# Optimization experiments

Measured on AMD Instinct MI355X. Metric: run time of the kernel, lower is better.

Reference implementation:

```python
import jax, jax.numpy as jnp
from jax import lax
import numpy as np

MAX_D = 4  # max_displacement


def conv3x3(x, w, b):
    # x: [B,Cin,H,W], w: [Cout,Cin,3,3], SAME padding (pad=1)
    y = lax.conv_general_dilated(
        x, w, window_strides=(1, 1), padding='SAME',
        dimension_numbers=('NCHW', 'OIHW', 'NCHW'))
    return y + b[None, :, None, None]


def compute_cost_volume(f1, f2, d):
    # roll+mask in the torch code == shift with zero padding:
    # cv[idx,h,w] = mean_c f1[c,h,w] * f2[c,h-i,w-j] (zero outside bounds)
    B, C, H, W = f1.shape
    pad = jnp.pad(f2, ((0, 0), (0, 0), (d, d), (d, d)))
    slices = []
    for i in range(-d, d + 1):
        for j in range(-d, d + 1):
            shifted = lax.dynamic_slice(pad, (0, 0, d - i, d - j), (B, C, H, W))
            slices.append((f1 * shifted).sum(axis=1) / C)  # [B,H,W]
    return jnp.stack(slices, axis=1)  # [B,81,H,W]


def setup_inputs() -> dict:
    key = jax.random.key(0)
    ks = jax.random.split(key, 10)
    B, C, H, W = 16, 64, 128, 128
    cv_ch = (2 * MAX_D + 1) ** 2  # 81
    def w_init(k, shape):
        fan_in = shape[1] * shape[2] * shape[3]
        return jax.random.normal(k, shape, dtype=jnp.float32) * np.float32(np.sqrt(2.0 / fan_in))
    return {
        'f1': jax.random.normal(ks[0], (B, C, H, W), dtype=jnp.float32),
        'f2_warped': jax.random.normal(ks[1], (B, C, H, W), dtype=jnp.float32),
        'w1': w_init(ks[2], (128, C + cv_ch, 3, 3)),
        'b1': jnp.zeros((128,), dtype=jnp.float32),
        'w2': w_init(ks[3], (64, 128, 3, 3)),
        'b2': jnp.zeros((64,), dtype=jnp.float32),
        'w3': w_init(ks[4], (32, 64, 3, 3)),
        'b3': jnp.zeros((32,), dtype=jnp.float32),
        'w4': w_init(ks[5], (2, 32, 3, 3)),
        'b4': jnp.zeros((2,), dtype=jnp.float32),
    }


def reference(f1, f2_warped, w1, b1, w2, b2, w3, b3, w4, b4):
    cv = compute_cost_volume(f1, f2_warped, MAX_D)       # [B,81,H,W]
    x = jnp.concatenate([f1, cv], axis=1)                # [B,145,H,W]
    x = jax.nn.relu(conv3x3(x, w1, b1))
    x = jax.nn.relu(conv3x3(x, w2, b2))
    x = jax.nn.relu(conv3x3(x, w3, b3))
    flow = conv3x3(x, w4, b4)                            # [B,2,H,W]
    return flow
```

## Files before the change

### kernel.cpp

```cpp
#include <hip/hip_runtime.h>


typedef __bf16 bf16x8 __attribute__((ext_vector_type(8)));
typedef float f32x4 __attribute__((ext_vector_type(4)));

__device__ __forceinline__ unsigned short f2bf_bits(float f) {
  unsigned int u = __float_as_uint(f);
  unsigned int r = (u + 0x7FFFu + ((u >> 16) & 1u)) >> 16;
  return (unsigned short)r;
}

__device__ __forceinline__ void glds16(const ushort* gp, ushort* lp) {
  __builtin_amdgcn_global_load_lds((const __attribute__((address_space(1))) void*)gp,
                                   (__attribute__((address_space(3))) void*)lp, 16, 0, 0);
}

__global__ void prep_w_kernel(const float* __restrict__ w, uint4* __restrict__ wp,
                              int CIN, int COUT, int CHUNKS, int NFRAG) {
  int idx = blockIdx.x * 256 + threadIdx.x;
  int total = CHUNKS * 9 * NFRAG * 64;
  if (idx >= total) return;
  int lane = idx & 63;
  int fi = idx >> 6;
  int nf = fi % NFRAG;
  int t = fi / NFRAG;
  int rs = t % 9;
  int c = t / 9;
  int co = nf * 16 + (lane & 15);
  int cib = c * 32 + (lane >> 4) * 8;
  union { uint4 q; ushort s[8]; } pk;
#pragma unroll
  for (int e = 0; e < 8; ++e) {
    int ci = cib + e;
    float v = (ci < CIN && co < COUT) ? w[(co * CIN + ci) * 9 + rs] : 0.f;
    pk.s[e] = f2bf_bits(v);
  }
  wp[idx] = pk.q;
}

__global__ __launch_bounds__(256) void pack_f1_kernel(const float* __restrict__ f1,
                                                      ushort* __restrict__ xf1) {
  __shared__ float tile[64][132];
  const int bid = blockIdx.x;
  const int h = bid & 127, b = bid >> 7;
  const int tid = threadIdx.x;
  for (int e = tid; e < 64 * 128; e += 256) {
    int c = e >> 7, w = e & 127;
    tile[c][w] = f1[((b * 64 + c) * 128 + h) * 128 + w];
  }
  __syncthreads();
  const int px = tid >> 1, cgb = (tid & 1) * 4;
  const long base = ((long)(b * 128 + h) * 128 + px) * 64;
#pragma unroll
  for (int e = 0; e < 4; ++e) {
    int c0 = (cgb + e) * 8;
    union { uint4 q; ushort s[8]; } pk;
#pragma unroll
    for (int k = 0; k < 8; ++k) pk.s[k] = f2bf_bits(tile[c0 + k][px]);
    *reinterpret_cast<uint4*>(&xf1[base + c0]) = pk.q;
  }
}

__global__ __launch_bounds__(256)
void cost_volume_kernel(const float* __restrict__ f1,
                        const float* __restrict__ f2,
                        ushort* __restrict__ xcv) {
  const int bx = blockIdx.x;
  const int idx = bx >> 3;
  const int b = 2 * (bx & 7) + (idx >> 6);
  const int h0 = (idx & 63) * 2;
  const int tid = threadIdx.x;
  const int q = tid & 31;
  const int rho = (tid >> 5) & 1;
  const int g = tid >> 6;

  __shared__ float arena[6464];

  float accF[2][9][4];
  float accP[3][4];
#pragma unroll
  for (int s = 0; s < 2; ++s)
#pragma unroll
    for (int jj = 0; jj < 9; ++jj)
#pragma unroll
      for (int e = 0; e < 4; ++e) accF[s][jj][e] = 0.f;
#pragma unroll
  for (int t = 0; t < 3; ++t)
#pragma unroll
    for (int e = 0; e < 4; ++e) accP[t][e] = 0.f;

  float st[13];

  auto stage = [&](int c) {
    const int cc = c * 2;
#pragma unroll
    for (int i = 0; i < 13; ++i) {
      int e = tid + i * 256;
      float v = 0.f;
      if (e < 2720) {
        int ci = e / 1360;
        int rem = e - ci * 1360;
        int a = rem / 136;
        int k = rem - a * 136;
        int gh = h0 - 4 + a, gw = k - 4;
        if ((unsigned)gh < 128u && (unsigned)gw < 128u)
          v = f2[((b * 64 + cc + ci) * 128 + gh) * 128 + gw];
      } else if (e < 3232) {
        int e2 = e - 2720;
        int ci = e2 >> 8, rr = (e2 >> 7) & 1, ww = e2 & 127;
        v = f1[((b * 64 + cc + ci) * 128 + h0 + rr) * 128 + ww];
      }
      st[i] = v;
    }
  };
  auto commit = [&](int bi) {
    float* bufp = arena + bi * 3232;
#pragma unroll
    for (int i = 0; i < 13; ++i) {
      int e = tid + i * 256;
      if (e < 3232) bufp[e] = st[i];
    }
  };

  stage(0);
  commit(0);

  for (int c = 0; c < 32; ++c) {
    __syncthreads();
    if (c < 31) stage(c + 1);
    const float* bufc = arena + (c & 1) * 3232;
#pragma unroll
    for (int ci = 0; ci < 2; ++ci) {
      const float* bp = bufc + ci * 1360;
      float4 f1q = *reinterpret_cast<const float4*>(bufc + 2720 + ci * 256 + rho * 128 + 4 * q);
      const float* f1e = &f1q.x;
#pragma unroll
      for (int s = 0; s < 2; ++s) {
        int a = rho + 8 - (2 * g + s);
        const float* rp = bp + a * 136 + 4 * q;
        float4 A = *reinterpret_cast<const float4*>(rp);
        float4 Bv = *reinterpret_cast<const float4*>(rp + 4);
        float4 Cv = *reinterpret_cast<const float4*>(rp + 8);
        float ev[12] = {A.x, A.y, A.z, A.w, Bv.x, Bv.y, Bv.z, Bv.w, Cv.x, Cv.y, Cv.z, Cv.w};
#pragma unroll
        for (int jj = 0; jj < 9; ++jj)
#pragma unroll
          for (int e = 0; e < 4; ++e)
            accF[s][jj][e] += f1e[e] * ev[8 - jj + e];
      }
      {
        const float* rp = bp + rho * 136 + 4 * q;
        if (g < 2) {
          float4 A = *reinterpret_cast<const float4*>(rp + 4);
          float4 Bv = *reinterpret_cast<const float4*>(rp + 8);
          float pv[8] = {A.x, A.y, A.z, A.w, Bv.x, Bv.y, Bv.z, Bv.w};
          if (g == 0) {
#pragma unroll
            for (int e = 0; e < 4; ++e) {
              accP[0][e] += f1e[e] * pv[4 + e];
              accP[1][e] += f1e[e] * pv[3 + e];
              accP[2][e] += f1e[e] * pv[2 + e];
            }
          } else {
#pragma unroll
            for (int e = 0; e < 4; ++e) {
              accP[0][e] += f1e[e] * pv[1 + e];
              accP[1][e] += f1e[e] * pv[e];
            }
          }
        } else {
          float4 A = *reinterpret_cast<const float4*>(rp);
          float4 Bv = *reinterpret_cast<const float4*>(rp + 4);
          float pv[8] = {A.x, A.y, A.z, A.w, Bv.x, Bv.y, Bv.z, Bv.w};
          if (g == 2) {
#pragma unroll
            for (int e = 0; e < 4; ++e) {
              accP[0][e] += f1e[e] * pv[3 + e];
              accP[1][e] += f1e[e] * pv[2 + e];
            }
          } else {
#pragma unroll
            for (int e = 0; e < 4; ++e) {
              accP[0][e] += f1e[e] * pv[1 + e];
              accP[1][e] += f1e[e] * pv[e];
            }
          }
        }
      }
    }
    if (c < 31) commit((c + 1) & 1);
  }

  ushort* sO = (ushort*)arena;
  const float inv = 1.0f / 64.0f;
#pragma unroll
  for (int r = 0; r < 2; ++r) {
    __syncthreads();
    if (rho == r) {
#pragma unroll
      for (int s = 0; s < 2; ++s) {
        int ch = (2 * g + s) * 9;
#pragma unroll
        for (int jj = 0; jj < 9; ++jj) {
          uint lo = (uint)f2bf_bits(accF[s][jj][0] * inv) | ((uint)f2bf_bits(accF[s][jj][1] * inv) << 16);
          uint hi = (uint)f2bf_bits(accF[s][jj][2] * inv) | ((uint)f2bf_bits(accF[s][jj][3] * inv) << 16);
          ushort* d = &sO[(ch + jj) * 132 + 4 * q];
          *reinterpret_cast<uint*>(d) = lo;
          *reinterpret_cast<uint*>(d + 2) = hi;
        }
      }
      const int npart = (g == 0) ? 3 : 2;
      const int chbase = 72 + ((g == 0) ? 0 : (g == 1) ? 3 : (g == 2) ? 5 : 7);
#pragma unroll
      for (int t = 0; t < 3; ++t) {
        if (t < npart) {
          uint lo = (uint)f2bf_bits(accP[t][0] * inv) | ((uint)f2bf_bits(accP[t][1] * inv) << 16);
          uint hi = (uint)f2bf_bits(accP[t][2] * inv) | ((uint)f2bf_bits(accP[t][3] * inv) << 16);
          ushort* d = &sO[(chbase + t) * 132 + 4 * q];
          *reinterpret_cast<uint*>(d) = lo;
          *reinterpret_cast<uint*>(d + 2) = hi;
        }
      }
    }
    if (r == 0) {
      for (int e = tid; e < 960; e += 256) {
        int ch = 81 + (e >> 6);
        int pxh = e & 63;
        *reinterpret_cast<uint*>(&sO[ch * 132 + pxh * 2]) = 0u;
      }
    }
    __syncthreads();
    uint4* dst = reinterpret_cast<uint4*>(xcv + ((long)(b * 128 + h0 + r) * 128) * 96);
#pragma unroll
    for (int j = 0; j < 6; ++j) {
      int t8 = 256 * j + tid;
      int px = t8 / 12;
      int ch0 = (t8 - px * 12) * 8;
      union { uint4 qq; ushort ss[8]; } pk;
#pragma unroll
      for (int k = 0; k < 8; ++k) pk.ss[k] = sO[(ch0 + k) * 132 + px];
      dst[t8] = pk.qq;
    }
  }
}

template <int CA, int CB, int COUT, bool RELU, bool PLANAR>
__global__ __launch_bounds__(512, 2)
void conv_mfma_kernel(const ushort* __restrict__ xa, const ushort* __restrict__ xb,
                      const uint4* __restrict__ wp, const float* __restrict__ bias,
                      void* __restrict__ outv) {
  constexpr int CHUNKS = (CA + CB) / 32;
  constexpr int NFRAG = COUT / 16;
  constexpr int NFW = (NFRAG >= 2) ? NFRAG / 2 : 1;
  constexpr int MFW = (NFRAG >= 2) ? 4 : 2;
  constexpr int SXN = 4 * 130 * 32;
  constexpr int WTQ = 9 * NFRAG * 64;
  constexpr int WI = (WTQ + 511) / 512;
  constexpr int SO_STRIDE = COUT + 4;
  constexpr int STAGE_B = PLANAR ? 2048 : 2 * 128 * SO_STRIDE * 2;
  constexpr int SX_B = 2 * SXN * 2;
  constexpr int BASE_B = SX_B + WTQ * 16;
  constexpr int ARENA_B = STAGE_B > BASE_B ? STAGE_B : BASE_B;

  __shared__ __align__(16) char arena[ARENA_B];
  ushort* sXa = (ushort*)arena;
  ushort* sWt = (ushort*)(arena + SX_B);

  const int bx = blockIdx.x;
  const int idx = bx >> 3;
  const int b = 2 * (bx & 7) + (idx >> 6);
  const int h0 = (idx & 63) * 2;
  const int tid = threadIdx.x;
  const int lane = tid & 63;
  const int wid = tid >> 6;
  const int l15 = lane & 15;
  const int lg = lane >> 4;
  const int cg    = (NFRAG >= 2) ? (wid >> 2) : 0;
  const int row   = (NFRAG >= 2) ? ((wid >> 1) & 1) : (wid >> 2);
  const int pbase = (NFRAG >= 2) ? ((wid & 1) * 64) : ((wid & 3) * 32);

  f32x4 acc[MFW][NFW];
#pragma unroll
  for (int mf = 0; mf < MFW; ++mf)
#pragma unroll
    for (int nf = 0; nf < NFW; ++nf) acc[mf][nf] = {0.f, 0.f, 0.f, 0.f};

  if (tid < 64) {
    int bi = tid >> 5, tr = (tid >> 3) & 3, wz = (tid >> 2) & 1, gq = tid & 3;
    int wl = wz ? 129 : 0;
    *reinterpret_cast<uint4*>(&sXa[bi * SXN + ((tr * 130 + wl) * 4 + gq) * 8]) =
        make_uint4(0u, 0u, 0u, 0u);
  }
  if (h0 == 0 || h0 == 126) {
    const int trz = (h0 == 0) ? 0 : 3;
#pragma unroll
    for (int e = 0; e < 2; ++e) {
      int u = tid + e * 512;
      int bi = u >> 9, k = u & 511;
      *reinterpret_cast<uint4*>(&sXa[bi * SXN + ((trz * 130 + 1) * 4 + k) * 8]) =
          make_uint4(0u, 0u, 0u, 0u);
    }
  }

  auto stage = [&](int c, int bi) {
    const int c0 = c * 32;
    const ushort* src;
    int cst, coff;
    if (CB == 0 || c0 < CA) { src = xa; cst = CA; coff = c0; }
    else                    { src = xb; cst = CB; coff = c0 - CA; }
    const int tr = wid >> 1;
    const int gh = h0 - 1 + tr;
    if ((unsigned)gh < 128u) {
      const ushort* rowp = src + ((long)(b * 128 + gh) * 128) * cst + coff;
#pragma unroll
      for (int t = 0; t < 4; ++t) {
        int s = (wid & 1) * 4 + t;
        int u = s * 64 + lane;
        int wl = 1 + (u >> 2);
        int gq = lane & 3;
        int sw = (wl + (wl >> 2)) & 3;
        const ushort* gp = rowp + (long)(wl - 1) * cst + (gq ^ sw) * 8;
        ushort* lp = &sXa[bi * SXN + ((tr * 130 + 1) * 4 + s * 64) * 8];
        glds16(gp, lp);
      }
    }
  };

  auto stage_wt = [&](int c) {
    const ushort* src = (const ushort*)(wp + (size_t)c * WTQ);
#pragma unroll
    for (int i = 0; i < WI; ++i) {
      int e = tid + i * 512;
      if ((WTQ & 511) == 0 || e < WTQ)
        glds16(src + e * 8, sWt + (size_t)(tid & ~63) * 8 + (size_t)(i * 512) * 8);
    }
  };

  stage(0, 0);
  stage_wt(0);
  __syncthreads();

  for (int c = 0; c < CHUNKS; ++c) {
    if (c + 1 < CHUNKS) stage(c + 1, (c + 1) & 1);
    const int bi = c & 1;
#pragma unroll
    for (int rs = 0; rs < 9; ++rs) {
      const int r = rs / 3, s = rs % 3;
      const int tr = row + r;
      bf16x8 afr[MFW];
#pragma unroll
      for (int mf = 0; mf < MFW; ++mf) {
        int wl = pbase + mf * 16 + l15 + s;
        int sw = (wl + (wl >> 2)) & 3;
        afr[mf] = *reinterpret_cast<const bf16x8*>(
            &sXa[bi * SXN + ((tr * 130 + wl) * 4 + (lg ^ sw)) * 8]);
      }
      const ushort* wrow = sWt + (size_t)(rs * NFRAG + cg * NFW) * 64 * 8;
#pragma unroll
      for (int nf = 0; nf < NFW; ++nf) {
        bf16x8 bfr = *reinterpret_cast<const bf16x8*>(wrow + (nf * 64 + lane) * 8);
#pragma unroll
        for (int mf = 0; mf < MFW; ++mf)
          acc[mf][nf] = __builtin_amdgcn_mfma_f32_16x16x32_bf16(afr[mf], bfr, acc[mf][nf], 0, 0, 0);
      }
    }
    __syncthreads();
    if (c + 1 < CHUNKS) stage_wt(c + 1);
    __syncthreads();
  }

  if (!PLANAR) {
    ushort* sO = (ushort*)arena;
#pragma unroll
    for (int nf = 0; nf < NFW; ++nf) {
      float bs = bias[cg * NFW * 16 + nf * 16 + l15];
#pragma unroll
      for (int mf = 0; mf < MFW; ++mf) {
        int px2 = row * 128 + pbase + mf * 16 + lg * 4;
#pragma unroll
        for (int j = 0; j < 4; ++j) {
          float v = acc[mf][nf][j] + bs;
          if (RELU) v = fmaxf(v, 0.f);
          sO[(px2 + j) * SO_STRIDE + cg * NFW * 16 + nf * 16 + l15] = f2bf_bits(v);
        }
      }
    }
    __syncthreads();
    constexpr int QPP = COUT / 8;
    uint4* dst = reinterpret_cast<uint4*>((ushort*)outv + ((long)(b * 128 + h0) * 128) * COUT);
#pragma unroll
    for (int t0 = 0; t0 < 2 * 128 * QPP / 512; ++t0) {
      int t = t0 * 512 + tid;
      int px2 = t / QPP;
      int ch0 = (t & (QPP - 1)) * 8;
      union { uint4 qq; ushort ss[8]; } pk;
#pragma unroll
      for (int k = 0; k < 8; ++k) pk.ss[k] = sO[px2 * SO_STRIDE + ch0 + k];
      dst[t] = pk.qq;
    }
  } else {
    float* sF = (float*)arena;
    if (l15 < 2) {
#pragma unroll
      for (int mf = 0; mf < MFW; ++mf) {
        int pxb = pbase + mf * 16 + lg * 4;
#pragma unroll
        for (int j = 0; j < 4; ++j)
          sF[(l15 * 2 + row) * 128 + pxb + j] = acc[mf][0][j] + bias[l15];
      }
    }
    __syncthreads();
    float* out = (float*)outv;
    if (tid < 128) {
      int ch = tid >> 6, r = (tid >> 5) & 1, qx = tid & 31;
      *reinterpret_cast<float4*>(&out[((long)(b * 2 + ch) * 128 + h0 + r) * 128 + qx * 4]) =
          *reinterpret_cast<float4*>(&sF[(ch * 2 + r) * 128 + qx * 4]);
    }
  }
}

extern "C" void kernel_launch(void* const* d_in, const int* in_sizes, int n_in,
                              void* d_out, int out_size, void* d_ws, size_t ws_size,
                              hipStream_t stream) {
  (void)in_sizes; (void)n_in; (void)out_size; (void)ws_size;
  const float* f1 = (const float*)d_in[0];
  const float* f2 = (const float*)d_in[1];
  const float* w1 = (const float*)d_in[2];
  const float* b1 = (const float*)d_in[3];
  const float* w2 = (const float*)d_in[4];
  const float* b2 = (const float*)d_in[5];
  const float* w3 = (const float*)d_in[6];
  const float* b3 = (const float*)d_in[7];
  const float* w4 = (const float*)d_in[8];
  const float* b4 = (const float*)d_in[9];

  char* ws = (char*)d_ws;
  size_t off = 0;
  ushort* xf1 = (ushort*)(ws + off); off += (size_t)262144 * 64 * 2;
  ushort* xcv = (ushort*)(ws + off); off += (size_t)262144 * 96 * 2;
  ushort* x1  = (ushort*)(ws + off); off += (size_t)262144 * 128 * 2;
  ushort* x2  = (ushort*)(ws + off); off += (size_t)262144 * 64 * 2;
  uint4* wp1 = (uint4*)(ws + off); off += (size_t)5 * 9 * 8 * 64 * 16;
  uint4* wp2 = (uint4*)(ws + off); off += (size_t)4 * 9 * 4 * 64 * 16;
  uint4* wp3 = (uint4*)(ws + off); off += (size_t)2 * 9 * 2 * 64 * 16;
  uint4* wp4 = (uint4*)(ws + off); off += (size_t)1 * 9 * 1 * 64 * 16;
  ushort* x3 = xf1;

  prep_w_kernel<<<90, 256, 0, stream>>>(w1, wp1, 145, 128, 5, 8);
  prep_w_kernel<<<36, 256, 0, stream>>>(w2, wp2, 128, 64, 4, 4);
  prep_w_kernel<<<9, 256, 0, stream>>>(w3, wp3, 64, 32, 2, 2);
  prep_w_kernel<<<3, 256, 0, stream>>>(w4, wp4, 32, 2, 1, 1);

  pack_f1_kernel<<<2048, 256, 0, stream>>>(f1, xf1);
  cost_volume_kernel<<<1024, 256, 0, stream>>>(f1, f2, xcv);

  conv_mfma_kernel<64, 96, 128, true, false><<<1024, 512, 0, stream>>>(xf1, xcv, wp1, b1, x1);
  conv_mfma_kernel<128, 0, 64, true, false><<<1024, 512, 0, stream>>>(x1, x1, wp2, b2, x2);
  conv_mfma_kernel<64, 0, 32, true, false><<<1024, 512, 0, stream>>>(x2, x2, wp3, b3, x3);
  conv_mfma_kernel<32, 0, 16, false, true><<<1024, 512, 0, stream>>>(x3, x3, wp4, b4, d_out);
}
```

Before: 335.4 us.

## Compute cost volume with bf16 MFMA on packed NHWC f1/f2

```diff
diff --git a/kernel.cpp b/kernel.cpp
--- a/kernel.cpp
+++ b/kernel.cpp
@@ -62,185 +62,99 @@
 }
 
 __global__ __launch_bounds__(256)
-void cost_volume_kernel(const float* __restrict__ f1,
-                        const float* __restrict__ f2,
-                        ushort* __restrict__ xcv) {
+void cost_volume_mfma_kernel(const ushort* __restrict__ xf1,
+                             const ushort* __restrict__ xf2,
+                             ushort* __restrict__ xcv) {
   const int bx = blockIdx.x;
   const int idx = bx >> 3;
-  const int b = 2 * (bx & 7) + (idx >> 6);
-  const int h0 = (idx & 63) * 2;
+  const int b = 2 * (bx & 7) + (idx >> 7);
+  const int h = idx & 127;
   const int tid = threadIdx.x;
-  const int q = tid & 31;
-  const int rho = (tid >> 5) & 1;
+  const int lane = tid & 63;
   const int g = tid >> 6;
-
-  __shared__ float arena[6464];
-
-  float accF[2][9][4];
-  float accP[3][4];
-#pragma unroll
-  for (int s = 0; s < 2; ++s)
-#pragma unroll
-    for (int jj = 0; jj < 9; ++jj)
-#pragma unroll
-      for (int e = 0; e < 4; ++e) accF[s][jj][e] = 0.f;
-#pragma unroll
-  for (int t = 0; t < 3; ++t)
-#pragma unroll
-    for (int e = 0; e < 4; ++e) accP[t][e] = 0.f;
-
-  float st[13];
-
-  auto stage = [&](int c) {
-    const int cc = c * 2;
-#pragma unroll
-    for (int i = 0; i < 13; ++i) {
-      int e = tid + i * 256;
-      float v = 0.f;
-      if (e < 2720) {
-        int ci = e / 1360;
-        int rem = e - ci * 1360;
-        int a = rem / 136;
-        int k = rem - a * 136;
-        int gh = h0 - 4 + a, gw = k - 4;
-        if ((unsigned)gh < 128u && (unsigned)gw < 128u)
-          v = f2[((b * 64 + cc + ci) * 128 + gh) * 128 + gw];
-      } else if (e < 3232) {
-        int e2 = e - 2720;
-        int ci = e2 >> 8, rr = (e2 >> 7) & 1, ww = e2 & 127;
-        v = f1[((b * 64 + cc + ci) * 128 + h0 + rr) * 128 + ww];
-      }
-      st[i] = v;
-    }
-  };
-  auto commit = [&](int bi) {
-    float* bufp = arena + bi * 3232;
-#pragma unroll
-    for (int i = 0; i < 13; ++i) {
-      int e = tid + i * 256;
-      if (e < 3232) bufp[e] = st[i];
-    }
-  };
-
-  stage(0);
-  commit(0);
-
-  for (int c = 0; c < 32; ++c) {
-    __syncthreads();
-    if (c < 31) stage(c + 1);
-    const float* bufc = arena + (c & 1) * 3232;
-#pragma unroll
-    for (int ci = 0; ci < 2; ++ci) {
-      const float* bp = bufc + ci * 1360;
-      float4 f1q = *reinterpret_cast<const float4*>(bufc + 2720 + ci * 256 + rho * 128 + 4 * q);
-      const float* f1e = &f1q.x;
-#pragma unroll
-      for (int s = 0; s < 2; ++s) {
-        int a = rho + 8 - (2 * g + s);
-        const float* rp = bp + a * 136 + 4 * q;
-        float4 A = *reinterpret_cast<const float4*>(rp);
-        float4 Bv = *reinterpret_cast<const float4*>(rp + 4);
-        float4 Cv = *reinterpret_cast<const float4*>(rp + 8);
-        float ev[12] = {A.x, A.y, A.z, A.w, Bv.x, Bv.y, Bv.z, Bv.w, Cv.x, Cv.y, Cv.z, Cv.w};
-#pragma unroll
-        for (int jj = 0; jj < 9; ++jj)
-#pragma unroll
-          for (int e = 0; e < 4; ++e)
-            accF[s][jj][e] += f1e[e] * ev[8 - jj + e];
-      }
-      {
-        const float* rp = bp + rho * 136 + 4 * q;
-        if (g < 2) {
-          float4 A = *reinterpret_cast<const float4*>(rp + 4);
-          float4 Bv = *reinterpret_cast<const float4*>(rp + 8);
-          float pv[8] = {A.x, A.y, A.z, A.w, Bv.x, Bv.y, Bv.z, Bv.w};
-          if (g == 0) {
-#pragma unroll
-            for (int e = 0; e < 4; ++e) {
-              accP[0][e] += f1e[e] * pv[4 + e];
-              accP[1][e] += f1e[e] * pv[3 + e];
-              accP[2][e] += f1e[e] * pv[2 + e];
-            }
-          } else {
-#pragma unroll
-            for (int e = 0; e < 4; ++e) {
-              accP[0][e] += f1e[e] * pv[1 + e];
-              accP[1][e] += f1e[e] * pv[e];
-            }
-          }
-        } else {
-          float4 A = *reinterpret_cast<const float4*>(rp);
-          float4 Bv = *reinterpret_cast<const float4*>(rp + 4);
-          float pv[8] = {A.x, A.y, A.z, A.w, Bv.x, Bv.y, Bv.z, Bv.w};
-          if (g == 2) {
-#pragma unroll
-            for (int e = 0; e < 4; ++e) {
-              accP[0][e] += f1e[e] * pv[3 + e];
-              accP[1][e] += f1e[e] * pv[2 + e];
-            }
-          } else {
-#pragma unroll
-            for (int e = 0; e < 4; ++e) {
-              accP[0][e] += f1e[e] * pv[1 + e];
-              accP[1][e] += f1e[e] * pv[e];
-            }
-          }
+  const int l15 = lane & 15;
+  const int lg = lane >> 4;
+
+  __shared__ __align__(16) float sC[4][2][16][33];
+  __shared__ __align__(16) ushort sO[96][132];
+
+  {
+    uint4 z = make_uint4(0u, 0u, 0u, 0u);
+    uint4* p = (uint4*)sO;
+#pragma unroll
+    for (int j = 0; j < 7; ++j) {
+      int e = tid + j * 256;
+      if (e < 1584) p[e] = z;
+    }
+  }
+  __syncthreads();
+
+  const int w0g = g * 32;
+  bf16x8 afr[2][2];
+  {
+    const ushort* f1p = xf1 + ((long)(b * 128 + h) * 128) * 64;
+#pragma unroll
+    for (int wt = 0; wt < 2; ++wt)
+#pragma unroll
+      for (int kc = 0; kc < 2; ++kc) {
+        int pix = w0g + wt * 16 + l15;
+        afr[wt][kc] = *reinterpret_cast<const bf16x8*>(f1p + pix * 64 + kc * 32 + lg * 8);
+      }
+  }
+
+  const float inv = 1.0f / 64.0f;
+  for (int A = 0; A < 9; ++A) {
+    int fr = h - 4 + A;
+    if ((unsigned)fr >= 128u) continue;
+    const ushort* f2p = xf2 + ((long)(b * 128 + fr) * 128) * 64;
+    bf16x8 bfr[3][2];
+#pragma unroll
+    for (int t = 0; t < 3; ++t)
+#pragma unroll
+      for (int kc = 0; kc < 2; ++kc) {
+        int p = w0g - 4 + t * 16 + l15;
+        uint4 v = make_uint4(0u, 0u, 0u, 0u);
+        if ((unsigned)p < 128u)
+          v = *reinterpret_cast<const uint4*>(f2p + (long)p * 64 + kc * 32 + lg * 8);
+        bfr[t][kc] = __builtin_bit_cast(bf16x8, v);
+      }
+#pragma unroll
+    for (int wt = 0; wt < 2; ++wt)
+#pragma unroll
+      for (int nt = 0; nt < 2; ++nt) {
+        f32x4 acc = {0.f, 0.f, 0.f, 0.f};
+        acc = __builtin_amdgcn_mfma_f32_16x16x32_bf16(afr[wt][0], bfr[wt + nt][0], acc, 0, 0, 0);
+        acc = __builtin_amdgcn_mfma_f32_16x16x32_bf16(afr[wt][1], bfr[wt + nt][1], acc, 0, 0, 0);
+#pragma unroll
+        for (int j = 0; j < 4; ++j)
+          sC[g][wt][lg * 4 + j][nt * 16 + l15] = acc[j];
+      }
+    const int chb = (8 - A) * 9;
+#pragma unroll
+    for (int wt = 0; wt < 2; ++wt) {
+      int px = w0g + wt * 16 + l15;
+#pragma unroll
+      for (int u = 0; u < 3; ++u) {
+        if (u < ((lg == 3) ? 3 : 2)) {
+          int tj = lg * 2 + u;
+          float v = sC[g][wt][l15][l15 + 8 - tj];
+          sO[chb + tj][px] = f2bf_bits(v * inv);
         }
       }
     }
-    if (c < 31) commit((c + 1) & 1);
-  }
-
-  ushort* sO = (ushort*)arena;
-  const float inv = 1.0f / 64.0f;
-#pragma unroll
-  for (int r = 0; r < 2; ++r) {
-    __syncthreads();
-    if (rho == r) {
-#pragma unroll
-      for (int s = 0; s < 2; ++s) {
-        int ch = (2 * g + s) * 9;
-#pragma unroll
-        for (int jj = 0; jj < 9; ++jj) {
-          uint lo = (uint)f2bf_bits(accF[s][jj][0] * inv) | ((uint)f2bf_bits(accF[s][jj][1] * inv) << 16);
-          uint hi = (uint)f2bf_bits(accF[s][jj][2] * inv) | ((uint)f2bf_bits(accF[s][jj][3] * inv) << 16);
-          ushort* d = &sO[(ch + jj) * 132 + 4 * q];
-          *reinterpret_cast<uint*>(d) = lo;
-          *reinterpret_cast<uint*>(d + 2) = hi;
-        }
-      }
-      const int npart = (g == 0) ? 3 : 2;
-      const int chbase = 72 + ((g == 0) ? 0 : (g == 1) ? 3 : (g == 2) ? 5 : 7);
-#pragma unroll
-      for (int t = 0; t < 3; ++t) {
-        if (t < npart) {
-          uint lo = (uint)f2bf_bits(accP[t][0] * inv) | ((uint)f2bf_bits(accP[t][1] * inv) << 16);
-          uint hi = (uint)f2bf_bits(accP[t][2] * inv) | ((uint)f2bf_bits(accP[t][3] * inv) << 16);
-          ushort* d = &sO[(chbase + t) * 132 + 4 * q];
-          *reinterpret_cast<uint*>(d) = lo;
-          *reinterpret_cast<uint*>(d + 2) = hi;
-        }
-      }
-    }
-    if (r == 0) {
-      for (int e = tid; e < 960; e += 256) {
-        int ch = 81 + (e >> 6);
-        int pxh = e & 63;
-        *reinterpret_cast<uint*>(&sO[ch * 132 + pxh * 2]) = 0u;
-      }
-    }
-    __syncthreads();
-    uint4* dst = reinterpret_cast<uint4*>(xcv + ((long)(b * 128 + h0 + r) * 128) * 96);
-#pragma unroll
-    for (int j = 0; j < 6; ++j) {
-      int t8 = 256 * j + tid;
-      int px = t8 / 12;
-      int ch0 = (t8 - px * 12) * 8;
-      union { uint4 qq; ushort ss[8]; } pk;
-#pragma unroll
-      for (int k = 0; k < 8; ++k) pk.ss[k] = sO[(ch0 + k) * 132 + px];
-      dst[t8] = pk.qq;
-    }
+  }
+  __syncthreads();
+
+  uint4* dst = reinterpret_cast<uint4*>(xcv + ((long)(b * 128 + h) * 128) * 96);
+#pragma unroll
+  for (int j = 0; j < 6; ++j) {
+    int t8 = j * 256 + tid;
+    int px = t8 / 12;
+    int ch0 = (t8 - px * 12) * 8;
+    union { uint4 qq; ushort ss[8]; } pk;
+#pragma unroll
+    for (int k = 0; k < 8; ++k) pk.ss[k] = sO[ch0 + k][px];
+    dst[t8] = pk.qq;
   }
 }
 
@@ -444,7 +358,8 @@
   uint4* wp2 = (uint4*)(ws + off); off += (size_t)4 * 9 * 4 * 64 * 16;
   uint4* wp3 = (uint4*)(ws + off); off += (size_t)2 * 9 * 2 * 64 * 16;
   uint4* wp4 = (uint4*)(ws + off); off += (size_t)1 * 9 * 1 * 64 * 16;
-  ushort* x3 = xf1;
+  ushort* x3  = xf1;
+  ushort* xf2 = x1;
 
   prep_w_kernel<<<90, 256, 0, stream>>>(w1, wp1, 145, 128, 5, 8);
   prep_w_kernel<<<36, 256, 0, stream>>>(w2, wp2, 128, 64, 4, 4);
@@ -452,7 +367,8 @@
   prep_w_kernel<<<3, 256, 0, stream>>>(w4, wp4, 32, 2, 1, 1);
 
   pack_f1_kernel<<<2048, 256, 0, stream>>>(f1, xf1);
-  cost_volume_kernel<<<1024, 256, 0, stream>>>(f1, f2, xcv);
+  pack_f1_kernel<<<2048, 256, 0, stream>>>(f2, xf2);
+  cost_volume_mfma_kernel<<<2048, 256, 0, stream>>>(xf1, xf2, xcv);
 
   conv_mfma_kernel<64, 96, 128, true, false><<<1024, 512, 0, stream>>>(xf1, xcv, wp1, b1, x1);
   conv_mfma_kernel<128, 0, 64, true, false><<<1024, 512, 0, stream>>>(x1, x1, wp2, b2, x2);
```

After: 322.2 us. 1.04x faster.
